# Kernel tuning notes

Measured on AMD Instinct MI355X. Metric: run time of the kernel, lower is better.

The kernel has to match this reference:

```python
import jax, jax.numpy as jnp
import numpy as np

BINS = jnp.array([1, 2, 3, 4, 8, 16, 32, 64], dtype=jnp.int32)
L = 10      # max span width
HID = 150   # Score hidden dim


def _mlp(x, W1, b1, W2, b2, W3, b3):
    # Score module: Linear -> ReLU -> Linear -> ReLU -> Linear (dropout = identity at eval)
    h = jax.nn.relu(x @ W1 + b1)
    h = jax.nn.relu(h @ W2 + b2)
    return h @ W3 + b3


def setup_inputs() -> dict:
    key = jax.random.key(0)
    ks = jax.random.split(key, 16)
    T, A, E, D, S = 8192, 1024, 512, 20, 32768
    GI = 2 * A + E + D  # 2580
    sc = lambda n: 1.0 / np.sqrt(n)
    return {
        "states": jax.random.normal(ks[0], (T, A), jnp.float32),
        "embeds": jax.random.normal(ks[1], (T, E), jnp.float32),
        "span_starts": jnp.sort(jax.random.randint(ks[2], (S,), 0, T - L)),
        "span_lengths": jax.random.randint(ks[3], (S,), 0, L),
        # attention Score params (attn_dim -> 150 -> 150 -> 1)
        "Wa1": jax.random.normal(ks[4], (A, HID), jnp.float32) * sc(A),
        "ba1": jnp.zeros((HID,), jnp.float32),
        "Wa2": jax.random.normal(ks[5], (HID, HID), jnp.float32) * sc(HID),
        "ba2": jnp.zeros((HID,), jnp.float32),
        "Wa3": jax.random.normal(ks[6], (HID, 1), jnp.float32) * sc(HID),
        "ba3": jnp.zeros((1,), jnp.float32),
        # Distance embedding table (len(bins)+1 = 9 buckets)
        "width_table": jax.random.normal(ks[7], (9, D), jnp.float32) * 0.1,
        # mention Score params (gi_dim -> 150 -> 150 -> 1)
        "Ws1": jax.random.normal(ks[8], (GI, HID), jnp.float32) * sc(GI),
        "bs1": jnp.zeros((HID,), jnp.float32),
        "Ws2": jax.random.normal(ks[9], (HID, HID), jnp.float32) * sc(HID),
        "bs2": jnp.zeros((HID,), jnp.float32),
        "Ws3": jax.random.normal(ks[10], (HID, 1), jnp.float32) * sc(HID),
        "bs3": jnp.zeros((1,), jnp.float32),
    }


def reference(states, embeds, span_starts, span_lengths,
              Wa1, ba1, Wa2, ba2, Wa3, ba3,
              width_table,
              Ws1, bs1, Ws2, bs2, Ws3, bs3):
    T = states.shape[0]
    # per-token attention logits: [T, 1]
    attns = _mlp(states, Wa1, ba1, Wa2, ba2, Wa3, ba3)

    pos = jnp.arange(L)
    idx = span_starts[:, None] + pos[None, :]                 # [S, L]
    mask = pos[None, :] <= span_lengths[:, None]              # valid positions
    idx = jnp.minimum(idx, T - 1)

    span_attn = jnp.where(mask, attns[idx, 0], -jnp.inf)      # [S, L]
    w = jax.nn.softmax(span_attn, axis=1)                     # per-span softmax
    pooled = jnp.einsum('sl,sle->se', w, embeds[idx])         # [S, E]

    ends = span_starts + span_lengths
    widths = span_lengths + 1
    bucket = jnp.searchsorted(BINS, widths.astype(jnp.int32), side='right')
    size_emb = width_table[bucket]                            # [S, D]

    g = jnp.concatenate([states[span_starts], states[ends], pooled, size_emb], axis=-1)
    scores = _mlp(g, Ws1, bs1, Ws2, bs2, Ws3, bs3)[:, 0]      # [S]
    return scores
```

## Files before the change

kernel.cpp:

```cpp
#include <hip/hip_runtime.h>
#include <math.h>

#define T_TOK 8192
#define A_DIM 1024
#define E_DIM 512
#define S_SPAN 32768
#define HID 150

typedef __attribute__((ext_vector_type(8))) short short8;
typedef __attribute__((ext_vector_type(4))) float f32x4;
typedef __attribute__((ext_vector_type(4))) unsigned int u32x4;

__device__ __forceinline__ unsigned short f2bf(float f) {
    unsigned int u = __builtin_bit_cast(unsigned int, f);
    u += 0x7FFFu + ((u >> 16) & 1u);
    return (unsigned short)(u >> 16);
}
__device__ __forceinline__ float bf2f(unsigned int h16) {
    unsigned int u = h16 << 16;
    return __builtin_bit_cast(float, u);
}
__device__ __forceinline__ short8 cast8(f32x4 a, f32x4 b) {
    short8 r;
    r[0] = (short)f2bf(a.x); r[1] = (short)f2bf(a.y);
    r[2] = (short)f2bf(a.z); r[3] = (short)f2bf(a.w);
    r[4] = (short)f2bf(b.x); r[5] = (short)f2bf(b.y);
    r[6] = (short)f2bf(b.z); r[7] = (short)f2bf(b.w);
    return r;
}

struct WConv { const float* src; unsigned short* dst; int K0; int Kpad; int nblk; };
struct PrepTab {
    WConv g[6];
    const float* wt; const float* Ws1w; const float* bs1; float* PW;
};

__global__ __launch_bounds__(256) void prep_kernel(PrepTab tab) {
    int b = blockIdx.x;
    #pragma unroll
    for (int gi = 0; gi < 6; ++gi) {
        if (b < tab.g[gi].nblk) {
            int idx = b * 256 + threadIdx.x;
            int Kpad = tab.g[gi].Kpad;
            if (idx < Kpad * 160) {
                int k = idx / 160, j = idx - k * 160;
                float v = (j < HID && k < tab.g[gi].K0)
                          ? tab.g[gi].src[(size_t)k * HID + j] : 0.f;
                tab.g[gi].dst[(size_t)j * Kpad + k] = f2bf(v);
            }
            return;
        }
        b -= tab.g[gi].nblk;
    }
    int j = threadIdx.x;
    if (j < 160) {
        float acc = 0.f;
        if (j < HID) {
            for (int k = 0; k < 20; ++k)
                acc = fmaf(tab.wt[b * 20 + k], tab.Ws1w[k * HID + j], acc);
            acc += tab.bs1[j];
        }
        tab.PW[b * 160 + j] = acc;
    }
}

struct GG {
    const void* A; int lda;
    const unsigned short* W; int K; int nrb;
    unsigned short* outh; int ldo;
    const float* bias; int relu;
    const float* dotv; const float* dotb; float* dotout;
    const unsigned short* W2; const float* bias2;
};
struct GTab { GG g[4]; int ng; };

template <int TAG, bool AF32>
__global__ __launch_bounds__(256) void gemm_fused(GTab tab) {
    constexpr int LDW = 72;
    __shared__ unsigned short WtL[2][160 * LDW];

    int b = blockIdx.x;
    int gi = 0;
    while (gi < tab.ng - 1 && b >= tab.g[gi].nrb) { b -= tab.g[gi].nrb; ++gi; }
    const GG G = tab.g[gi];

    const int tid = threadIdx.x;
    const int wid = tid >> 6;
    const int lane = tid & 63;
    const int l15 = lane & 15;
    const int quad = lane >> 4;
    const int row0 = b * 64 + wid * 16 + l15;
    const int K = G.K;
    const int nch = K >> 6;
    const float* Af = (const float*)G.A + (size_t)row0 * G.lda;
    const unsigned short* Ah = (const unsigned short*)G.A + (size_t)row0 * G.lda;

    int sn[5], sk[5];
    #pragma unroll
    for (int i = 0; i < 5; ++i) { int u = tid + i * 256; sn[i] = u >> 3; sk[i] = (u & 7) * 8; }

    f32x4 acc[10];
    #pragma unroll
    for (int nt = 0; nt < 10; ++nt) acc[nt] = (f32x4){0.f, 0.f, 0.f, 0.f};

    u32x4 wA[5], wB[5];
    f32x4 fAa[4], fAb[4];
    short8 hAa[2], hAb[2];
    short8 avc0, avc1;

#define LOAD_W(SET, KOFF)                                                     \
    {   _Pragma("unroll")                                                     \
        for (int i = 0; i < 5; ++i)                                           \
            SET[i] = *(const u32x4*)(G.W + (size_t)sn[i] * K + (KOFF) + sk[i]); }
#define LOAD_A(FSET, HSET, KOFF)                                              \
    if (AF32) {                                                               \
        FSET[0] = *(const f32x4*)(Af + (KOFF) + quad * 8);                    \
        FSET[1] = *(const f32x4*)(Af + (KOFF) + quad * 8 + 4);                \
        FSET[2] = *(const f32x4*)(Af + (KOFF) + 32 + quad * 8);               \
        FSET[3] = *(const f32x4*)(Af + (KOFF) + 32 + quad * 8 + 4);           \
    } else {                                                                  \
        HSET[0] = *(const short8*)(Ah + (KOFF) + quad * 8);                   \
        HSET[1] = *(const short8*)(Ah + (KOFF) + 32 + quad * 8);              \
    }
#define STORE_W(SET, BUF)                                                     \
    {   _Pragma("unroll")                                                     \
        for (int i = 0; i < 5; ++i)                                           \
            *(u32x4*)&WtL[BUF][sn[i] * LDW + sk[i]] = SET[i]; }
#define SET_AVC(FSET, HSET)                                                   \
    if (AF32) { avc0 = cast8(FSET[0], FSET[1]); avc1 = cast8(FSET[2], FSET[3]); } \
    else      { avc0 = HSET[0]; avc1 = HSET[1]; }
#define MFMA_BLOCK(BUF)                                                       \
    {   _Pragma("unroll")                                                     \
        for (int nt = 0; nt < 10; ++nt) {                                     \
            short8 bv0 = *(const short8*)&WtL[BUF][(nt * 16 + l15) * LDW + quad * 8]; \
            acc[nt] = __builtin_amdgcn_mfma_f32_16x16x32_bf16(avc0, bv0, acc[nt], 0, 0, 0); \
            short8 bv1 = *(const short8*)&WtL[BUF][(nt * 16 + l15) * LDW + 32 + quad * 8]; \
            acc[nt] = __builtin_amdgcn_mfma_f32_16x16x32_bf16(avc1, bv1, acc[nt], 0, 0, 0); \
        } }

    LOAD_W(wA, 0);
    LOAD_A(fAa, hAa, 0);
    LOAD_W(wB, 64);
    LOAD_A(fAb, hAb, 64);
    STORE_W(wA, 0);
    SET_AVC(fAa, hAa);
    __syncthreads();

    for (int c = 0; c < nch; c += 2) {
        const bool mA = (c + 2 < nch);
        if (mA) {
            const int kn = (c + 2) << 6;
            LOAD_W(wA, kn);
            LOAD_A(fAa, hAa, kn);
        }
        STORE_W(wB, 1);
        MFMA_BLOCK(0);
        SET_AVC(fAb, hAb);
        __syncthreads();

        const bool mB = (c + 3 < nch);
        if (mB) {
            const int kn = (c + 3) << 6;
            LOAD_W(wB, kn);
            LOAD_A(fAb, hAb, kn);
        }
        if (mA) STORE_W(wA, 0);
        MFMA_BLOCK(1);
        if (mA) SET_AVC(fAa, hAa);
        __syncthreads();
    }

#undef LOAD_W
#undef LOAD_A
#undef STORE_W
#undef SET_AVC
#undef MFMA_BLOCK

    const int rbase = b * 64 + wid * 16 + quad * 4;
    if (G.W2) {
        constexpr int LDH = 168;
        unsigned short* tile = &WtL[0][0] + wid * 16 * LDH;
        #pragma unroll
        for (int nt = 0; nt < 10; ++nt) {
            int col = nt * 16 + l15;
            float bv_ = (col < HID) ? G.bias[col] : 0.f;
            #pragma unroll
            for (int r = 0; r < 4; ++r) {
                float v = fmaxf(acc[nt][r] + bv_, 0.f);
                tile[(quad * 4 + r) * LDH + col] = f2bf(v);
            }
        }
        f32x4 acc2[10];
        #pragma unroll
        for (int nt = 0; nt < 10; ++nt) acc2[nt] = (f32x4){0.f, 0.f, 0.f, 0.f};
        #pragma unroll
        for (int kc = 0; kc < 5; ++kc) {
            short8 av = *(const short8*)&tile[l15 * LDH + kc * 32 + quad * 8];
            #pragma unroll
            for (int nt = 0; nt < 10; ++nt) {
                short8 bv = *(const short8*)(G.W2 + (size_t)(nt * 16 + l15) * 192 + kc * 32 + quad * 8);
                acc2[nt] = __builtin_amdgcn_mfma_f32_16x16x32_bf16(av, bv, acc2[nt], 0, 0, 0);
            }
        }
        float part[4] = {0.f, 0.f, 0.f, 0.f};
        #pragma unroll
        for (int nt = 0; nt < 10; ++nt) {
            int col = nt * 16 + l15;
            float b2 = (col < HID) ? G.bias2[col] : 0.f;
            float vv = (col < HID) ? G.dotv[col] : 0.f;
            #pragma unroll
            for (int r = 0; r < 4; ++r)
                part[r] += fmaxf(acc2[nt][r] + b2, 0.f) * vv;
        }
        #pragma unroll
        for (int r = 0; r < 4; ++r) {
            float p = part[r];
            #pragma unroll
            for (int off = 1; off < 16; off <<= 1) p += __shfl_xor(p, off);
            if (l15 == 0) G.dotout[rbase + r] = p + G.dotb[0];
        }
    } else if (G.dotout) {
        float part[4] = {0.f, 0.f, 0.f, 0.f};
        #pragma unroll
        for (int nt = 0; nt < 10; ++nt) {
            int col = nt * 16 + l15;
            float bv_ = (col < HID) ? G.bias[col] : 0.f;
            float vv = (col < HID) ? G.dotv[col] : 0.f;
            #pragma unroll
            for (int r = 0; r < 4; ++r)
                part[r] += fmaxf(acc[nt][r] + bv_, 0.f) * vv;
        }
        #pragma unroll
        for (int r = 0; r < 4; ++r) {
            float p = part[r];
            #pragma unroll
            for (int off = 1; off < 16; off <<= 1) p += __shfl_xor(p, off);
            if (l15 == 0) G.dotout[rbase + r] = p + G.dotb[0];
        }
    } else {
        #pragma unroll
        for (int nt = 0; nt < 10; ++nt) {
            int col = nt * 16 + l15;
            float bv_ = (G.bias != nullptr && col < HID) ? G.bias[col] : 0.f;
            #pragma unroll
            for (int r = 0; r < 4; ++r) {
                int row = rbase + r;
                float v = acc[nt][r] + bv_;
                if (G.relu) v = fmaxf(v, 0.f);
                G.outh[(size_t)row * G.ldo + col] = f2bf(v);
            }
        }
    }
}

__device__ __forceinline__ void add_bf8(f32x4& A, f32x4& B, u32x4 u) {
    A.x += bf2f(u.x & 0xffff); A.y += bf2f(u.x >> 16);
    A.z += bf2f(u.y & 0xffff); A.w += bf2f(u.y >> 16);
    B.x += bf2f(u.z & 0xffff); B.y += bf2f(u.z >> 16);
    B.z += bf2f(u.w & 0xffff); B.w += bf2f(u.w >> 16);
}
__device__ __forceinline__ void fma_bf8(f32x4& A, f32x4& B, u32x4 u, float w) {
    A.x = fmaf(w, bf2f(u.x & 0xffff), A.x); A.y = fmaf(w, bf2f(u.x >> 16), A.y);
    A.z = fmaf(w, bf2f(u.y & 0xffff), A.z); A.w = fmaf(w, bf2f(u.y >> 16), A.w);
    B.x = fmaf(w, bf2f(u.z & 0xffff), B.x); B.y = fmaf(w, bf2f(u.z >> 16), B.y);
    B.z = fmaf(w, bf2f(u.w & 0xffff), B.z); B.w = fmaf(w, bf2f(u.w >> 16), B.w);
}

__global__ __launch_bounds__(256) void span_fused_kernel(
        const float* __restrict__ attns,
        const int* __restrict__ starts,
        const int* __restrict__ lens,
        const unsigned short* __restrict__ Ps,
        const unsigned short* __restrict__ Pe,
        const unsigned short* __restrict__ Pm,
        const float* __restrict__ PW,
        const unsigned short* __restrict__ W2,
        const float* __restrict__ bs2,
        const float* __restrict__ Ws3,
        const float* __restrict__ bs3,
        float* __restrict__ out) {
    constexpr int LDH = 200;
    __shared__ unsigned short tileAll[4][16 * LDH];
    const int wid = threadIdx.x >> 6;
    const int lane = threadIdx.x & 63;
    const int r = lane & 15;
    const int q = lane >> 4;
    unsigned short* tile = &tileAll[wid][0];
    const int s = blockIdx.x * 64 + wid * 16 + r;

    const int start = starts[s];
    const int len = lens[s];
    const int end = start + len;
    const int width = len + 1;
    const int bucket = (width >= 1) + (width >= 2) + (width >= 3) + (width >= 4) +
                       (width >= 8) + (width >= 16) + (width >= 32) + (width >= 64);

    int il[10];
    float wgt[10];
    float m = -INFINITY;
    #pragma unroll
    for (int l = 0; l < 10; ++l) {
        int iv = min(start + l, T_TOK - 1);
        il[l] = iv * 160;
        wgt[l] = (l <= len) ? attns[iv] : -INFINITY;
        m = fmaxf(m, wgt[l]);
    }
    float ssum = 0.f;
    #pragma unroll
    for (int l = 0; l < 10; ++l) { wgt[l] = __expf(wgt[l] - m); ssum += wgt[l]; }
    const float inv = 1.f / ssum;
    #pragma unroll
    for (int l = 0; l < 10; ++l) wgt[l] *= inv;

    const unsigned short* ps = Ps + (size_t)start * 160;
    const unsigned short* pe = Pe + (size_t)end * 160;
    const float* pw = PW + bucket * 160;

    #pragma unroll
    for (int i = 0; i < 5; ++i) {
        const int j0 = (q + 4 * i) * 8;
        f32x4 a0 = *(const f32x4*)(pw + j0);
        f32x4 a1 = *(const f32x4*)(pw + j0 + 4);
        add_bf8(a0, a1, *(const u32x4*)(ps + j0));
        add_bf8(a0, a1, *(const u32x4*)(pe + j0));
        #pragma unroll
        for (int l = 0; l < 10; ++l)
            fma_bf8(a0, a1, *(const u32x4*)(Pm + il[l] + j0), wgt[l]);
        u32x4 pk;
        pk.x = (unsigned)f2bf(fmaxf(a0.x, 0.f)) | ((unsigned)f2bf(fmaxf(a0.y, 0.f)) << 16);
        pk.y = (unsigned)f2bf(fmaxf(a0.z, 0.f)) | ((unsigned)f2bf(fmaxf(a0.w, 0.f)) << 16);
        pk.z = (unsigned)f2bf(fmaxf(a1.x, 0.f)) | ((unsigned)f2bf(fmaxf(a1.y, 0.f)) << 16);
        pk.w = (unsigned)f2bf(fmaxf(a1.z, 0.f)) | ((unsigned)f2bf(fmaxf(a1.w, 0.f)) << 16);
        *(u32x4*)&tile[r * LDH + j0] = pk;
    }

    f32x4 acc[10];
    #pragma unroll
    for (int nt = 0; nt < 10; ++nt) acc[nt] = (f32x4){0.f, 0.f, 0.f, 0.f};
    #pragma unroll
    for (int kc = 0; kc < 5; ++kc) {
        short8 av = *(const short8*)&tile[r * LDH + kc * 32 + q * 8];
        #pragma unroll
        for (int nt = 0; nt < 10; ++nt) {
            short8 bv = *(const short8*)(W2 + (size_t)(nt * 16 + r) * 192 + kc * 32 + q * 8);
            acc[nt] = __builtin_amdgcn_mfma_f32_16x16x32_bf16(av, bv, acc[nt], 0, 0, 0);
        }
    }

    float part[4] = {0.f, 0.f, 0.f, 0.f};
    #pragma unroll
    for (int nt = 0; nt < 10; ++nt) {
        int col = nt * 16 + r;
        float b2 = (col < HID) ? bs2[col] : 0.f;
        float vv = (col < HID) ? Ws3[col] : 0.f;
        #pragma unroll
        for (int rr = 0; rr < 4; ++rr)
            part[rr] += fmaxf(acc[nt][rr] + b2, 0.f) * vv;
    }
    const int rbase = blockIdx.x * 64 + wid * 16 + q * 4;
    #pragma unroll
    for (int rr = 0; rr < 4; ++rr) {
        float p = part[rr];
        #pragma unroll
        for (int off = 1; off < 16; off <<= 1) p += __shfl_xor(p, off);
        if (r == 0) out[rbase + rr] = p + bs3[0];
    }
}

extern "C" void kernel_launch(void* const* d_in, const int* in_sizes, int n_in,
                              void* d_out, int out_size, void* d_ws, size_t ws_size,
                              hipStream_t stream) {
    const float* states = (const float*)d_in[0];
    const float* embeds = (const float*)d_in[1];
    const int* span_starts = (const int*)d_in[2];
    const int* span_lengths = (const int*)d_in[3];
    const float* Wa1 = (const float*)d_in[4];
    const float* ba1 = (const float*)d_in[5];
    const float* Wa2 = (const float*)d_in[6];
    const float* ba2 = (const float*)d_in[7];
    const float* Wa3 = (const float*)d_in[8];
    const float* ba3 = (const float*)d_in[9];
    const float* width_table = (const float*)d_in[10];
    const float* Ws1 = (const float*)d_in[11];
    const float* bs1 = (const float*)d_in[12];
    const float* Ws2 = (const float*)d_in[13];
    const float* bs2 = (const float*)d_in[14];
    const float* Ws3 = (const float*)d_in[15];
    const float* bs3 = (const float*)d_in[16];
    float* out = (float*)d_out;

    char* w = (char*)d_ws;
    unsigned short* WtA  = (unsigned short*)w;  w += 480 * 1024 * 2;
    unsigned short* WtE  = (unsigned short*)w;  w += 160 * 512 * 2;
    unsigned short* Wa2t = (unsigned short*)w;  w += 160 * 192 * 2;
    unsigned short* Ws2t = (unsigned short*)w;  w += 160 * 192 * 2;
    float* PW    = (float*)w;                   w += 9 * 160 * 4;
    float* attns = (float*)w;                   w += 8192 * 4;
    unsigned short* Psh = (unsigned short*)w;   w += (size_t)T_TOK * 160 * 2;
    unsigned short* Peh = (unsigned short*)w;   w += (size_t)T_TOK * 160 * 2;
    unsigned short* Pmh = (unsigned short*)w;   w += (size_t)T_TOK * 160 * 2;

    PrepTab pt;
    pt.g[0] = { Wa1,              WtA,              1024, 1024, (160*1024 + 255)/256 };
    pt.g[1] = { Ws1,              WtA + 160*1024,   1024, 1024, (160*1024 + 255)/256 };
    pt.g[2] = { Ws1 + 1024*150,   WtA + 320*1024,   1024, 1024, (160*1024 + 255)/256 };
    pt.g[3] = { Ws1 + 2048*150,   WtE,               512,  512, (160*512  + 255)/256 };
    pt.g[4] = { Wa2,              Wa2t,              150,  192, (160*192  + 255)/256 };
    pt.g[5] = { Ws2,              Ws2t,              150,  192, (160*192  + 255)/256 };
    pt.wt = width_table; pt.Ws1w = Ws1 + 2560*150; pt.bs1 = bs1; pt.PW = PW;
    int wblk = 0; for (int i = 0; i < 6; ++i) wblk += pt.g[i].nblk;
    prep_kernel<<<wblk + 9, 256, 0, stream>>>(pt);

    GG z = {};

    GTab t1; t1.ng = 4;
    t1.g[0] = z; t1.g[0].A = states; t1.g[0].lda = 1024; t1.g[0].W = WtA;            t1.g[0].K = 1024;
    t1.g[0].nrb = 128; t1.g[0].bias = ba1;
    t1.g[0].W2 = Wa2t; t1.g[0].bias2 = ba2;
    t1.g[0].dotv = Wa3; t1.g[0].dotb = ba3; t1.g[0].dotout = attns;
    t1.g[1] = z; t1.g[1].A = states; t1.g[1].lda = 1024; t1.g[1].W = WtA + 160*1024; t1.g[1].K = 1024;
    t1.g[1].nrb = 128; t1.g[1].outh = Psh; t1.g[1].ldo = 160;
    t1.g[2] = z; t1.g[2].A = states; t1.g[2].lda = 1024; t1.g[2].W = WtA + 320*1024; t1.g[2].K = 1024;
    t1.g[2].nrb = 128; t1.g[2].outh = Peh; t1.g[2].ldo = 160;
    t1.g[3] = z; t1.g[3].A = embeds; t1.g[3].lda = 512;  t1.g[3].W = WtE;            t1.g[3].K = 512;
    t1.g[3].nrb = 128; t1.g[3].outh = Pmh; t1.g[3].ldo = 160;
    gemm_fused<1, true><<<512, 256, 0, stream>>>(t1);

    span_fused_kernel<<<S_SPAN / 64, 256, 0, stream>>>(attns, span_starts, span_lengths,
                                                       Psh, Peh, Pmh, PW, Ws2t,
                                                       bs2, Ws3, bs3, out);
}
```

Measured before the change: 177.0 us.

## Tile weight transpose through LDS and use lighter barrier in GEMM loop

The weight conversion kernel now transposes 64x64 tiles through padded shared memory, so both the fp32 reads and the bf16 writes are coalesced instead of writing with a stride of Kpad. Grid sizing is changed to three 64-wide column tiles per 64-row K tile. Separately, the GEMM main loop replaces __syncthreads with a custom barrier that waits only on LDS counters (lgkmcnt) before s_barrier, so in-flight global prefetch loads are no longer drained at each sync. The custom barrier relies on the global loads being complete before their registers are used, which the compiler must still enforce.

After: 172.9 us. 2.3% less time.

```diff
diff --git a/kernel.cpp b/kernel.cpp
--- a/kernel.cpp
+++ b/kernel.cpp
@@ -29,6 +29,14 @@
     return r;
 }
 
+__device__ __forceinline__ void pub_barrier() {
+    __builtin_amdgcn_sched_barrier(0);
+    asm volatile("s_waitcnt lgkmcnt(0)" ::: "memory");
+    __builtin_amdgcn_sched_barrier(0);
+    __builtin_amdgcn_s_barrier();
+    __builtin_amdgcn_sched_barrier(0);
+}
+
 struct WConv { const float* src; unsigned short* dst; int K0; int Kpad; int nblk; };
 struct PrepTab {
     WConv g[6];
@@ -36,17 +44,32 @@
 };
 
 __global__ __launch_bounds__(256) void prep_kernel(PrepTab tab) {
+    __shared__ float tl[64][65];
     int b = blockIdx.x;
     #pragma unroll
     for (int gi = 0; gi < 6; ++gi) {
         if (b < tab.g[gi].nblk) {
-            int idx = b * 256 + threadIdx.x;
-            int Kpad = tab.g[gi].Kpad;
-            if (idx < Kpad * 160) {
-                int k = idx / 160, j = idx - k * 160;
-                float v = (j < HID && k < tab.g[gi].K0)
-                          ? tab.g[gi].src[(size_t)k * HID + j] : 0.f;
-                tab.g[gi].dst[(size_t)j * Kpad + k] = f2bf(v);
+            const int kt   = tab.g[gi].Kpad >> 6;
+            const int j0   = (b / kt) * 64;
+            const int k0   = (b % kt) * 64;
+            const int K0   = tab.g[gi].K0;
+            const int Kpad = tab.g[gi].Kpad;
+            const int ty = threadIdx.x >> 6, tx = threadIdx.x & 63;
+            const float* src = tab.g[gi].src;
+            #pragma unroll
+            for (int r = 0; r < 16; ++r) {
+                int k = k0 + ty * 16 + r;
+                int j = j0 + tx;
+                tl[ty * 16 + r][tx] = (j < HID && k < K0)
+                                      ? src[(size_t)k * HID + j] : 0.f;
+            }
+            __syncthreads();
+            unsigned short* dst = tab.g[gi].dst;
+            #pragma unroll
+            for (int r = 0; r < 16; ++r) {
+                int j = j0 + ty * 16 + r;
+                if (j < 160)
+                    dst[(size_t)j * Kpad + k0 + tx] = f2bf(tl[tx][ty * 16 + r]);
             }
             return;
         }
@@ -144,7 +167,7 @@
     LOAD_A(fAb, hAb, 64);
     STORE_W(wA, 0);
     SET_AVC(fAa, hAa);
-    __syncthreads();
+    pub_barrier();
 
     for (int c = 0; c < nch; c += 2) {
         const bool mA = (c + 2 < nch);
@@ -156,7 +179,7 @@
         STORE_W(wB, 1);
         MFMA_BLOCK(0);
         SET_AVC(fAb, hAb);
-        __syncthreads();
+        pub_barrier();
 
         const bool mB = (c + 3 < nch);
         if (mB) {
@@ -167,7 +190,7 @@
         if (mA) STORE_W(wA, 0);
         MFMA_BLOCK(1);
         if (mA) SET_AVC(fAa, hAa);
-        __syncthreads();
+        pub_barrier();
     }
 
 #undef LOAD_W
@@ -401,12 +424,12 @@
     unsigned short* Pmh = (unsigned short*)w;   w += (size_t)T_TOK * 160 * 2;
 
     PrepTab pt;
-    pt.g[0] = { Wa1,              WtA,              1024, 1024, (160*1024 + 255)/256 };
-    pt.g[1] = { Ws1,              WtA + 160*1024,   1024, 1024, (160*1024 + 255)/256 };
-    pt.g[2] = { Ws1 + 1024*150,   WtA + 320*1024,   1024, 1024, (160*1024 + 255)/256 };
-    pt.g[3] = { Ws1 + 2048*150,   WtE,               512,  512, (160*512  + 255)/256 };
-    pt.g[4] = { Wa2,              Wa2t,              150,  192, (160*192  + 255)/256 };
-    pt.g[5] = { Ws2,              Ws2t,              150,  192, (160*192  + 255)/256 };
+    pt.g[0] = { Wa1,              WtA,              1024, 1024, 3 * (1024/64) };
+    pt.g[1] = { Ws1,              WtA + 160*1024,   1024, 1024, 3 * (1024/64) };
+    pt.g[2] = { Ws1 + 1024*150,   WtA + 320*1024,   1024, 1024, 3 * (1024/64) };
+    pt.g[3] = { Ws1 + 2048*150,   WtE,               512,  512, 3 * (512/64)  };
+    pt.g[4] = { Wa2,              Wa2t,              150,  192, 3 * (192/64)  };
+    pt.g[5] = { Ws2,              Ws2t,              150,  192, 3 * (192/64)  };
     pt.wt = width_table; pt.Ws1w = Ws1 + 2560*150; pt.bs1 = bs1; pt.PW = PW;
     int wblk = 0; for (int i = 0; i < 6; ++i) wblk += pt.g[i].nblk;
     prep_kernel<<<wblk + 9, 256, 0, stream>>>(pt);
```
